# Optimization experiments

Measured on AMD Instinct MI355X. Metric: run time of the kernel, lower is better.

## Reference

```python
import jax, jax.numpy as jnp
import numpy as np

BS, C_IN, CTX, TGT = 2, 8, 1024, 96
D_MODEL, N_HEADS, D_FF, N_LAYERS = 256, 16, 1024, 4
PF, SF, PC, SC = 8, 4, 32, 16
NF = (CTX + SF - PF) // SF + 1   # 256 fine patches (incl. end-pad)
NC = (CTX + SC - PC) // SC + 1   # 64 coarse patches
TOTAL = NF + NC                  # 320
EPS = 1e-5
DK = D_MODEL // N_HEADS
SCALE = DK ** -0.5


def _patchify(z, plen, stride):
    # ReplicationPad1d((0, stride)) then unfold -> (bs, c, n_patches, plen)
    pad = jnp.broadcast_to(z[..., -1:], z.shape[:-1] + (stride,))
    zp = jnp.concatenate([z, pad], axis=-1)
    n = (zp.shape[-1] - plen) // stride + 1
    idx = np.arange(n)[:, None] * stride + np.arange(plen)[None, :]
    return zp[..., idx]


def _layernorm(x, s, b):
    m = x.mean(-1, keepdims=True)
    v = jnp.var(x, axis=-1, keepdims=True)
    return (x - m) * jax.lax.rsqrt(v + EPS) * s + b


def setup_inputs() -> dict:
    key = jax.random.key(0)
    ks = jax.random.split(key, 16)
    g = lambda k, shape: jax.random.normal(k, shape, jnp.float32) * 0.02
    return {
        "z": jax.random.normal(ks[0], (BS, C_IN, CTX), jnp.float32),
        "revin_w": jnp.ones((C_IN,), jnp.float32),
        "revin_b": jnp.zeros((C_IN,), jnp.float32),
        "Wf": g(ks[1], (PF, D_MODEL)), "bf": jnp.zeros((D_MODEL,), jnp.float32),
        "Wc": g(ks[2], (PC, D_MODEL)), "bc": jnp.zeros((D_MODEL,), jnp.float32),
        "W_pos": jax.random.uniform(ks[3], (TOTAL, D_MODEL), jnp.float32, -0.02, 0.02),
        "WQ": g(ks[4], (N_LAYERS, D_MODEL, D_MODEL)), "bQ": jnp.zeros((N_LAYERS, D_MODEL), jnp.float32),
        "WK": g(ks[5], (N_LAYERS, D_MODEL, D_MODEL)), "bK": jnp.zeros((N_LAYERS, D_MODEL), jnp.float32),
        "WV": g(ks[6], (N_LAYERS, D_MODEL, D_MODEL)), "bV": jnp.zeros((N_LAYERS, D_MODEL), jnp.float32),
        "WO": g(ks[7], (N_LAYERS, D_MODEL, D_MODEL)), "bO": jnp.zeros((N_LAYERS, D_MODEL), jnp.float32),
        "ln1_s": jnp.ones((N_LAYERS, D_MODEL), jnp.float32), "ln1_b": jnp.zeros((N_LAYERS, D_MODEL), jnp.float32),
        "ln2_s": jnp.ones((N_LAYERS, D_MODEL), jnp.float32), "ln2_b": jnp.zeros((N_LAYERS, D_MODEL), jnp.float32),
        "F1": g(ks[8], (N_LAYERS, D_MODEL, D_FF)), "c1": jnp.zeros((N_LAYERS, D_FF), jnp.float32),
        "F2": g(ks[9], (N_LAYERS, D_FF, D_MODEL)), "c2": jnp.zeros((N_LAYERS, D_MODEL), jnp.float32),
        "Wh": g(ks[10], (D_MODEL * TOTAL, TGT)), "bh": jnp.zeros((TGT,), jnp.float32),
    }


def reference(z, revin_w, revin_b, Wf, bf, Wc, bc, W_pos, WQ, bQ, WK, bK, WV, bV,
              WO, bO, ln1_s, ln1_b, ln2_s, ln2_b, F1, c1, F2, c2, Wh, bh):
    # RevIN norm over the time axis (last axis of (bs, c, T))
    mean = z.mean(-1, keepdims=True)
    std = jnp.sqrt(jnp.var(z, axis=-1, keepdims=True) + EPS)
    zn = (z - mean) / std * revin_w[None, :, None] + revin_b[None, :, None]

    # dual-scale patch embedding
    x_fine = _patchify(zn, PF, SF) @ Wf + bf      # (bs, c, NF, d)
    x_coarse = _patchify(zn, PC, SC) @ Wc + bc    # (bs, c, NC, d)
    x = jnp.concatenate([x_fine, x_coarse], axis=2)  # (bs, c, TOTAL, d)

    u = x.reshape(BS * C_IN, TOTAL, D_MODEL) + W_pos  # (B, S, d), B=bs*c

    # residual-score transformer encoder (post-norm)
    prev = None
    for l in range(N_LAYERS):
        q = (u @ WQ[l] + bQ[l]).reshape(-1, TOTAL, N_HEADS, DK).transpose(0, 2, 1, 3)
        k = (u @ WK[l] + bK[l]).reshape(-1, TOTAL, N_HEADS, DK).transpose(0, 2, 1, 3)
        v = (u @ WV[l] + bV[l]).reshape(-1, TOTAL, N_HEADS, DK).transpose(0, 2, 1, 3)
        s = jnp.einsum('bhqd,bhkd->bhqk', q, k) * SCALE
        if prev is not None:
            s = s + prev
        w = jax.nn.softmax(s, axis=-1)
        o = jnp.einsum('bhqk,bhkd->bhqd', w, v).transpose(0, 2, 1, 3).reshape(-1, TOTAL, D_MODEL)
        o = o @ WO[l] + bO[l]
        u = _layernorm(u + o, ln1_s[l], ln1_b[l])
        h = jax.nn.gelu(u @ F1[l] + c1[l], approximate=False) @ F2[l] + c2[l]
        u = _layernorm(u + h, ln2_s[l], ln2_b[l])
        prev = s

    # head: (bs, c, TOTAL, d) -> permute -> flatten(d, TOTAL) -> linear
    zz = u.reshape(BS, C_IN, TOTAL, D_MODEL).transpose(0, 1, 3, 2).reshape(BS, C_IN, D_MODEL * TOTAL)
    out = zz @ Wh + bh  # (bs, c, TGT)

    # RevIN denorm
    out = (out - revin_b[None, :, None]) / (revin_w[None, :, None] + EPS * EPS) * std + mean
    return out
```

## Files before the change

kernel.cpp:

```cpp
#include <hip/hip_runtime.h>
#include <math.h>

typedef unsigned short ushort;
typedef unsigned int uint;
typedef __attribute__((ext_vector_type(8))) short short8;
typedef __attribute__((ext_vector_type(4))) float f32x4;
typedef __attribute__((ext_vector_type(4))) ushort us4;

constexpr int BS = 2, C_IN = 8, CTX = 1024, TGT = 96;
constexpr int DM = 256, NH = 16, DFF = 1024, NL = 4;
constexpr int NF = 256, TOTAL = 320;
constexpr int NB = 16;
constexpr int DK = 16;
constexpr float EPS = 1e-5f;
constexpr float SCALE = 0.25f;
constexpr int KHEAD = DM * TOTAL;
constexpr int M = NB * TOTAL;

__device__ __forceinline__ ushort f2b(float x) {
    uint u = __float_as_uint(x);
    u += 0x7fff + ((u >> 16) & 1);
    return (ushort)(u >> 16);
}
__device__ __forceinline__ float bu2f(ushort x) { return __uint_as_float(((uint)x) << 16); }
__device__ __forceinline__ float lo2f(uint p) { return __uint_as_float(p << 16); }
__device__ __forceinline__ float hi2f(uint p) { return __uint_as_float(p & 0xffff0000u); }
__device__ __forceinline__ uint pack2(float a, float b) { return (uint)f2b(a) | ((uint)f2b(b) << 16); }

__global__ void k_convt(const float* __restrict__ src, ushort* __restrict__ dst,
                        int R, int C, int sls, int dls) {
    __shared__ ushort tile[32][33];
    src += (size_t)blockIdx.z * sls;
    dst += (size_t)blockIdx.z * dls;
    int c0 = blockIdx.x * 32, r0 = blockIdx.y * 32;
    int tx = threadIdx.x, ty = threadIdx.y;
    tile[ty][tx] = f2b(src[(r0 + ty) * C + c0 + tx]);
    __syncthreads();
    dst[(c0 + ty) * R + r0 + tx] = tile[tx][ty];
}

__global__ void k_convt_sq(const float* __restrict__ WQ, const float* __restrict__ WK,
                           const float* __restrict__ WV, const float* __restrict__ WO,
                           ushort* __restrict__ Wtqkv, ushort* __restrict__ WtO) {
    __shared__ ushort tile[32][33];
    int z = blockIdx.z, w = z >> 2, l = z & 3;
    const float* src = (w == 0 ? WQ : (w == 1 ? WK : (w == 2 ? WV : WO))) + l * 65536;
    ushort* dst = (w < 3) ? (Wtqkv + (size_t)l * 768 * 256 + w * 256 * 256)
                          : (WtO + (size_t)l * 65536);
    int c0 = blockIdx.x * 32, r0 = blockIdx.y * 32;
    int tx = threadIdx.x, ty = threadIdx.y;
    tile[ty][tx] = f2b(src[(r0 + ty) * 256 + c0 + tx]);
    __syncthreads();
    dst[(c0 + ty) * 256 + r0 + tx] = tile[tx][ty];
}

__global__ void k_convt_head(const float* __restrict__ Wh, ushort* __restrict__ WhT2) {
    __shared__ ushort tile[32][33];
    int t0 = blockIdx.x * 32, d0 = blockIdx.y * 32, p = blockIdx.z;
    int tx = threadIdx.x, ty = threadIdx.y;
    tile[ty][tx] = f2b(Wh[((size_t)(d0 + ty) * 320 + p) * 96 + t0 + tx]);
    __syncthreads();
    WhT2[(size_t)(t0 + ty) * KHEAD + p * 256 + d0 + tx] = tile[tx][ty];
}

__global__ void k_revin(const float* __restrict__ z, const float* __restrict__ rw,
                        const float* __restrict__ rb, float* __restrict__ zn,
                        float* __restrict__ meanv, float* __restrict__ stdv) {
    int bc = blockIdx.x, t = threadIdx.x;
    __shared__ float r1[256], r2[256];
    float s1 = 0.f, s2 = 0.f;
    for (int i = t; i < CTX; i += 256) {
        float x = z[bc * CTX + i];
        s1 += x; s2 += x * x;
    }
    r1[t] = s1; r2[t] = s2; __syncthreads();
    for (int off = 128; off > 0; off >>= 1) {
        if (t < off) { r1[t] += r1[t + off]; r2[t] += r2[t + off]; }
        __syncthreads();
    }
    float m = r1[0] * (1.0f / CTX);
    float var = r2[0] * (1.0f / CTX) - m * m;
    float sd = sqrtf(var + EPS);
    float w = rw[bc % C_IN], b = rb[bc % C_IN];
    float inv = 1.0f / sd;
    for (int i = t; i < CTX; i += 256) {
        float x = z[bc * CTX + i];
        zn[bc * CTX + i] = (x - m) * inv * w + b;
    }
    if (t == 0) { meanv[bc] = m; stdv[bc] = sd; }
}

__global__ void k_embed(const float* __restrict__ zn, const float* __restrict__ Wf,
                        const float* __restrict__ bfv, const float* __restrict__ Wc,
                        const float* __restrict__ bcv, const float* __restrict__ Wpos,
                        ushort* __restrict__ u) {
    int bc = blockIdx.x / TOTAL, p = blockIdx.x % TOTAL, d = threadIdx.x;
    float acc;
    if (p < NF) {
        acc = bfv[d];
        int base = p * 4;
        for (int i = 0; i < 8; i++) {
            int idx = min(base + i, CTX - 1);
            acc += zn[bc * CTX + idx] * Wf[i * DM + d];
        }
    } else {
        int pc = p - NF;
        acc = bcv[d];
        int base = pc * 16;
        for (int i = 0; i < 32; i++) {
            int idx = min(base + i, CTX - 1);
            acc += zn[bc * CTX + idx] * Wc[i * DM + d];
        }
    }
    acc += Wpos[p * DM + d];
    u[(bc * TOTAL + p) * DM + d] = f2b(acc);
}

template <int GELU, int QKV>
__global__ __launch_bounds__(256) void k_gemm_mfma(const ushort* __restrict__ A,
                                                   const ushort* __restrict__ Wt,
                                                   const float* __restrict__ b0,
                                                   const float* __restrict__ b1,
                                                   const float* __restrict__ b2,
                                                   ushort* __restrict__ C,
                                                   int Mm, int N, int K) {
    __shared__ ushort As[64][40];
    __shared__ ushort Bs[64][40];
    int tid = threadIdx.x;
    int wave = tid >> 6, lane = tid & 63;
    int quad = lane >> 4, l16 = lane & 15;
    int m0 = blockIdx.y * 64, n0 = blockIdx.x * 64;

    f32x4 acc[4];
#pragma unroll
    for (int nt = 0; nt < 4; nt++) acc[nt] = (f32x4){0.f, 0.f, 0.f, 0.f};

    int row = tid >> 2, kc = (tid & 3) * 8;
    for (int k0 = 0; k0 < K; k0 += 32) {
        *(short8*)&As[row][kc] = *(const short8*)&A[(m0 + row) * K + k0 + kc];
        *(short8*)&Bs[row][kc] = *(const short8*)&Wt[(n0 + row) * K + k0 + kc];
        __syncthreads();
        short8 af = *(const short8*)&As[wave * 16 + l16][quad * 8];
#pragma unroll
        for (int nt = 0; nt < 4; nt++) {
            short8 bf = *(const short8*)&Bs[nt * 16 + l16][quad * 8];
            acc[nt] = __builtin_amdgcn_mfma_f32_16x16x32_bf16(af, bf, acc[nt], 0, 0, 0);
        }
        __syncthreads();
    }
#pragma unroll
    for (int nt = 0; nt < 4; nt++) {
        int col = n0 + nt * 16 + l16;
        float bi;
        if (QKV) {
            int bs = (n0 + nt * 16) >> 8;
            const float* bp = bs == 0 ? b0 : (bs == 1 ? b1 : b2);
            bi = bp[col & 255];
        } else {
            bi = b0[col];
        }
#pragma unroll
        for (int r = 0; r < 4; r++) {
            int rowm = m0 + wave * 16 + quad * 4 + r;
            float vv = acc[nt][r] + bi;
            if (GELU) vv = vv * 0.5f * (1.0f + erff(vv * 0.70710678118f));
            if (QKV) C[(col >> 8) * (M * DM) + rowm * DM + (col & 255)] = f2b(vv);
            else C[rowm * N + col] = f2b(vv);
        }
    }
}

__global__ __launch_bounds__(256, 4) void k_attn(const ushort* __restrict__ qm, const ushort* __restrict__ km,
                                                 const ushort* __restrict__ vm, uint4* __restrict__ sp,
                                                 ushort* __restrict__ ao, int mode) {
    __shared__ ushort sh[10240];
    uint* sh32 = (uint*)sh;
    int bh = blockIdx.x, b = bh >> 4, h = bh & 15;
    int i0 = blockIdx.y * 64;
    int t = threadIdx.x, wave = t >> 6, lane = t & 63, quad = lane >> 4, l16 = lane & 15;
    const short8 zero8 = (short8){0, 0, 0, 0, 0, 0, 0, 0};

    for (int idx = t; idx < 640; idx += 256) {
        int j = idx >> 1, half = idx & 1;
        short8 kv = *(const short8*)&km[(b * TOTAL + j) * DM + h * DK + half * 8];
        int jt = j >> 4, jl = j & 15;
        *(short8*)&sh[((jt * 2 + half) * 16 + jl) * 8] = kv;
    }
    for (int idx = t; idx < 320; idx += 256) {
        int jp = idx >> 1, dh = idx & 1;
        int j = jp * 2;
        uint4 a = *(const uint4*)&vm[(b * TOTAL + j) * DM + h * DK + dh * 8];
        uint4 bb = *(const uint4*)&vm[(b * TOTAL + j + 1) * DM + h * DK + dh * 8];
        const ushort* ap = (const ushort*)&a;
        const ushort* bp = (const ushort*)&bb;
        int jr = j & 31;
        int q = (jr & 15) >> 2, jj = ((jr >> 4) << 2) + (jr & 3);
        int base = 5120 + ((j >> 5) * 4 + q) * 128 + jj;
#pragma unroll
        for (int dd = 0; dd < 8; dd++) {
            int d = dh * 8 + dd;
            uint val = (uint)ap[dd] | ((uint)bp[dd] << 16);
            sh32[(base + d * 8) >> 1] = val;
        }
    }
    short8 qf = zero8;
    if (quad < 2) qf = *(const short8*)&qm[(b * TOTAL + i0 + wave * 16 + l16) * DM + h * DK + quad * 8];
    __syncthreads();

    f32x4 acc[20];
#pragma unroll
    for (int nt = 0; nt < 20; nt++) {
        short8 kf = *(const short8*)&sh[((nt * 2 + (quad & 1)) * 16 + l16) * 8];
        acc[nt] = __builtin_amdgcn_mfma_f32_16x16x32_bf16(kf, qf, (f32x4){0.f, 0.f, 0.f, 0.f}, 0, 0, 0);
    }

    int cb = (bh * 5 + (int)blockIdx.y) * 10 * 256 + t;
#pragma unroll
    for (int c = 0; c < 10; c++) {
        float e[8];
#pragma unroll
        for (int j = 0; j < 8; j++) e[j] = acc[2 * c + (j >> 2)][j & 3] * SCALE;
        if (mode) {
            uint4 pv = sp[cb + c * 256];
            e[0] += lo2f(pv.x); e[1] += hi2f(pv.x); e[2] += lo2f(pv.y); e[3] += hi2f(pv.y);
            e[4] += lo2f(pv.z); e[5] += hi2f(pv.z); e[6] += lo2f(pv.w); e[7] += hi2f(pv.w);
        }
        if (mode != 2) {
            uint4 ov;
            ov.x = pack2(e[0], e[1]); ov.y = pack2(e[2], e[3]);
            ov.z = pack2(e[4], e[5]); ov.w = pack2(e[6], e[7]);
            sp[cb + c * 256] = ov;
        }
#pragma unroll
        for (int j = 0; j < 8; j++) acc[2 * c + (j >> 2)][j & 3] = e[j];
    }

    float mx = -1e30f;
#pragma unroll
    for (int nt = 0; nt < 20; nt++)
#pragma unroll
        for (int r = 0; r < 4; r++) mx = fmaxf(mx, acc[nt][r]);
    mx = fmaxf(mx, __shfl_xor(mx, 16));
    mx = fmaxf(mx, __shfl_xor(mx, 32));
    float sum = 0.f;
#pragma unroll
    for (int nt = 0; nt < 20; nt++)
#pragma unroll
        for (int r = 0; r < 4; r++) { acc[nt][r] = __expf(acc[nt][r] - mx); sum += acc[nt][r]; }
    sum += __shfl_xor(sum, 16);
    sum += __shfl_xor(sum, 32);
    float inv = 1.f / sum;
#pragma unroll
    for (int nt = 0; nt < 20; nt++)
#pragma unroll
        for (int r = 0; r < 4; r++) acc[nt][r] *= inv;

    f32x4 oacc = (f32x4){0.f, 0.f, 0.f, 0.f};
#pragma unroll
    for (int jt2 = 0; jt2 < 10; jt2++) {
        short8 vt = *(const short8*)&sh[5120 + ((jt2 * 4 + quad) * 16 + l16) * 8];
        union { short8 v; uint u[4]; } pf;
        pf.u[0] = pack2(acc[2 * jt2][0], acc[2 * jt2][1]);
        pf.u[1] = pack2(acc[2 * jt2][2], acc[2 * jt2][3]);
        pf.u[2] = pack2(acc[2 * jt2 + 1][0], acc[2 * jt2 + 1][1]);
        pf.u[3] = pack2(acc[2 * jt2 + 1][2], acc[2 * jt2 + 1][3]);
        oacc = __builtin_amdgcn_mfma_f32_16x16x32_bf16(vt, pf.v, oacc, 0, 0, 0);
    }
    us4 ov4 = (us4){f2b(oacc[0]), f2b(oacc[1]), f2b(oacc[2]), f2b(oacc[3])};
    *(us4*)&ao[(b * TOTAL + i0 + wave * 16 + l16) * DM + h * DK + quad * 4] = ov4;
}

__global__ __launch_bounds__(256) void k_add_ln(ushort* __restrict__ u, const ushort* __restrict__ o,
                                                const float* __restrict__ ls, const float* __restrict__ lb) {
    int wave = threadIdx.x >> 6, lane = threadIdx.x & 63;
    int row = blockIdx.x * 4 + wave;
    int d0 = lane * 4;
    uint2 uv = *(const uint2*)&u[row * DM + d0];
    uint2 ov = *(const uint2*)&o[row * DM + d0];
    float x0 = lo2f(uv.x) + lo2f(ov.x);
    float x1 = hi2f(uv.x) + hi2f(ov.x);
    float x2 = lo2f(uv.y) + lo2f(ov.y);
    float x3 = hi2f(uv.y) + hi2f(ov.y);
    float sum = x0 + x1 + x2 + x3;
    float sq = x0 * x0 + x1 * x1 + x2 * x2 + x3 * x3;
#pragma unroll
    for (int off = 1; off < 64; off <<= 1) {
        sum += __shfl_xor(sum, off);
        sq += __shfl_xor(sq, off);
    }
    float m = sum * (1.0f / DM);
    float var = sq * (1.0f / DM) - m * m;
    float rs = rsqrtf(var + EPS);
    f32x4 sc = *(const f32x4*)&ls[d0];
    f32x4 bb = *(const f32x4*)&lb[d0];
    float y0 = (x0 - m) * rs * sc[0] + bb[0];
    float y1 = (x1 - m) * rs * sc[1] + bb[1];
    float y2 = (x2 - m) * rs * sc[2] + bb[2];
    float y3 = (x3 - m) * rs * sc[3] + bb[3];
    uint2 w;
    w.x = pack2(y0, y1); w.y = pack2(y2, y3);
    *(uint2*)&u[row * DM + d0] = w;
}

__global__ __launch_bounds__(256) void k_head(const ushort* __restrict__ u, const ushort* __restrict__ WhT2,
                                              float* __restrict__ acc_head) {
    int t0 = blockIdx.x * 16;
    int wave = threadIdx.x >> 6, lane = threadIdx.x & 63;
    int quad = lane >> 4, l16 = lane & 15;
    int kbeg = (blockIdx.y * 4 + wave) * 1024;
    f32x4 acc = (f32x4){0.f, 0.f, 0.f, 0.f};
    const ushort* za = &u[(size_t)l16 * KHEAD + quad * 8];
    const ushort* wb = &WhT2[(size_t)(t0 + l16) * KHEAD + quad * 8];
#pragma unroll 4
    for (int k = kbeg; k < kbeg + 1024; k += 32) {
        short8 af = *(const short8*)&za[k];
        short8 bf = *(const short8*)&wb[k];
        acc = __builtin_amdgcn_mfma_f32_16x16x32_bf16(af, bf, acc, 0, 0, 0);
    }
#pragma unroll
    for (int r = 0; r < 4; r++)
        atomicAdd(&acc_head[(quad * 4 + r) * TGT + t0 + l16], acc[r]);
}

__global__ void k_final(const float* __restrict__ acc_head, const float* __restrict__ bh,
                        const float* __restrict__ rw, const float* __restrict__ rb,
                        const float* __restrict__ meanv, const float* __restrict__ stdv,
                        float* __restrict__ out) {
    int idx = blockIdx.x * 256 + threadIdx.x;
    if (idx >= NB * TGT) return;
    int bc = idx / TGT, t = idx % TGT, c = bc % C_IN;
    float vv = acc_head[idx] + bh[t];
    vv = (vv - rb[c]) / (rw[c] + EPS * EPS) * stdv[bc] + meanv[bc];
    out[idx] = vv;
}

extern "C" void kernel_launch(void* const* d_in, const int* in_sizes, int n_in,
                              void* d_out, int out_size, void* d_ws, size_t ws_size,
                              hipStream_t stream) {
    const float* z       = (const float*)d_in[0];
    const float* revin_w = (const float*)d_in[1];
    const float* revin_b = (const float*)d_in[2];
    const float* Wf      = (const float*)d_in[3];
    const float* bfv     = (const float*)d_in[4];
    const float* Wc      = (const float*)d_in[5];
    const float* bcv     = (const float*)d_in[6];
    const float* Wpos    = (const float*)d_in[7];
    const float* WQ      = (const float*)d_in[8];
    const float* bQ      = (const float*)d_in[9];
    const float* WK      = (const float*)d_in[10];
    const float* bK      = (const float*)d_in[11];
    const float* WV      = (const float*)d_in[12];
    const float* bV      = (const float*)d_in[13];
    const float* WO      = (const float*)d_in[14];
    const float* bO      = (const float*)d_in[15];
    const float* ln1s    = (const float*)d_in[16];
    const float* ln1b    = (const float*)d_in[17];
    const float* ln2s    = (const float*)d_in[18];
    const float* ln2b    = (const float*)d_in[19];
    const float* F1      = (const float*)d_in[20];
    const float* c1      = (const float*)d_in[21];
    const float* F2      = (const float*)d_in[22];
    const float* c2      = (const float*)d_in[23];
    const float* Wh      = (const float*)d_in[24];
    const float* bh      = (const float*)d_in[25];
    float* out = (float*)d_out;

    char* p = (char*)d_ws;
    float* meanv = (float*)p;    p += 16 * 4;
    float* stdv  = (float*)p;    p += 16 * 4;
    float* acc_head = (float*)p; p += NB * TGT * 4;
    p = (char*)(((size_t)p + 255) & ~255ull);
    float* zn = (float*)p;       p += NB * CTX * 4;
    ushort* u    = (ushort*)p;   p += (size_t)M * DM * 2;
    ushort* qkv  = (ushort*)p;   p += (size_t)3 * M * DM * 2;
    ushort* ax   = (ushort*)p;   p += (size_t)M * DM * 2;
    ushort* o    = (ushort*)p;   p += (size_t)M * DM * 2;
    ushort* hbuf = (ushort*)p;   p += (size_t)M * DFF * 2;
    ushort* Wtqkv = (ushort*)p;  p += (size_t)NL * 768 * 256 * 2;
    ushort* WtO   = (ushort*)p;  p += (size_t)NL * 256 * 256 * 2;
    ushort* Ft1   = (ushort*)p;  p += (size_t)NL * 1024 * 256 * 2;
    ushort* Ft2   = (ushort*)p;  p += (size_t)NL * 256 * 1024 * 2;
    ushort* WhT2  = (ushort*)p;  p += (size_t)TGT * KHEAD * 2;
    p = (char*)(((size_t)p + 255) & ~255ull);
    uint4* sp = (uint4*)p;       p += (size_t)NB * NH * 5 * 10 * 256 * 16;

    k_convt_sq<<<dim3(8, 8, 16), dim3(32, 32), 0, stream>>>(WQ, WK, WV, WO, Wtqkv, WtO);
    k_convt<<<dim3(32, 8, 4), dim3(32, 32), 0, stream>>>(F1, Ft1, 256, 1024, 262144, 262144);
    k_convt<<<dim3(8, 32, 4), dim3(32, 32), 0, stream>>>(F2, Ft2, 1024, 256, 262144, 262144);
    k_convt_head<<<dim3(3, 8, 320), dim3(32, 32), 0, stream>>>(Wh, WhT2);

    k_revin<<<NB, 256, 0, stream>>>(z, revin_w, revin_b, zn, meanv, stdv);
    k_embed<<<NB * TOTAL, 256, 0, stream>>>(zn, Wf, bfv, Wc, bcv, Wpos, u);

    for (int l = 0; l < NL; l++) {
        int mode = (l == 0) ? 0 : (l == NL - 1 ? 2 : 1);
        k_gemm_mfma<0, 1><<<dim3(12, 80), 256, 0, stream>>>(
            u, Wtqkv + (size_t)l * 768 * 256, bQ + l * DM, bK + l * DM, bV + l * DM, qkv, M, 768, 256);
        k_attn<<<dim3(NB * NH, 5), 256, 0, stream>>>(qkv, qkv + M * DM, qkv + 2 * M * DM, sp, ax, mode);
        k_gemm_mfma<0, 0><<<dim3(4, 80), 256, 0, stream>>>(
            ax, WtO + (size_t)l * 65536, bO + l * DM, bO + l * DM, bO + l * DM, o, M, 256, 256);
        k_add_ln<<<M / 4, 256, 0, stream>>>(u, o, ln1s + l * DM, ln1b + l * DM);
        k_gemm_mfma<1, 0><<<dim3(16, 80), 256, 0, stream>>>(
            u, Ft1 + (size_t)l * 262144, c1 + l * DFF, c1, c1, hbuf, M, 1024, 256);
        k_gemm_mfma<0, 0><<<dim3(4, 80), 256, 0, stream>>>(
            hbuf, Ft2 + (size_t)l * 262144, c2 + l * DM, c2, c2, o, M, 256, 1024);
        k_add_ln<<<M / 4, 256, 0, stream>>>(u, o, ln2s + l * DM, ln2b + l * DM);
    }

    hipMemsetAsync(acc_head, 0, NB * TGT * sizeof(float), stream);
    k_head<<<dim3(TGT / 16, 20), 256, 0, stream>>>(u, WhT2, acc_head);
    k_final<<<(NB * TGT + 255) / 256, 256, 0, stream>>>(acc_head, bh, revin_w, revin_b, meanv, stdv, out);
}
```

Before: 498.3 us.

## Fuse output/FFN2 GEMMs with residual LayerNorm and merge weight prep kernels

Adds a GEMM kernel that computes a full 16-row by 256-column tile per block, then applies bias, the residual add and LayerNorm in the epilogue, replacing the separate GEMM plus add_ln pair after attention and after the FFN. The four weight transpose/convert kernels are merged into one launch, attention mode becomes a template parameter, and the head's atomics plus memset are replaced by per-chunk partial sums reduced in k_final. This cuts kernel launches and the round trip of the intermediate output buffer. The cost is that the fused GEMM runs only 320 blocks, each reloading the whole weight panel per K step, which may lower GEMM efficiency, especially for the K=1024 FFN2.

```diff
diff --git a/kernel.cpp b/kernel.cpp
--- a/kernel.cpp
+++ b/kernel.cpp
@@ -27,40 +27,49 @@
 __device__ __forceinline__ float hi2f(uint p) { return __uint_as_float(p & 0xffff0000u); }
 __device__ __forceinline__ uint pack2(float a, float b) { return (uint)f2b(a) | ((uint)f2b(b) << 16); }
 
-__global__ void k_convt(const float* __restrict__ src, ushort* __restrict__ dst,
-                        int R, int C, int sls, int dls) {
+__global__ void k_prep(const float* __restrict__ WQ, const float* __restrict__ WK,
+                       const float* __restrict__ WV, const float* __restrict__ WO,
+                       const float* __restrict__ F1, const float* __restrict__ F2,
+                       const float* __restrict__ Wh,
+                       ushort* __restrict__ Wtqkv, ushort* __restrict__ WtO,
+                       ushort* __restrict__ Ft1, ushort* __restrict__ Ft2,
+                       ushort* __restrict__ WhT2) {
     __shared__ ushort tile[32][33];
-    src += (size_t)blockIdx.z * sls;
-    dst += (size_t)blockIdx.z * dls;
-    int c0 = blockIdx.x * 32, r0 = blockIdx.y * 32;
+    int i = blockIdx.x;
     int tx = threadIdx.x, ty = threadIdx.y;
-    tile[ty][tx] = f2b(src[(r0 + ty) * C + c0 + tx]);
-    __syncthreads();
-    dst[(c0 + ty) * R + r0 + tx] = tile[tx][ty];
-}
-
-__global__ void k_convt_sq(const float* __restrict__ WQ, const float* __restrict__ WK,
-                           const float* __restrict__ WV, const float* __restrict__ WO,
-                           ushort* __restrict__ Wtqkv, ushort* __restrict__ WtO) {
-    __shared__ ushort tile[32][33];
-    int z = blockIdx.z, w = z >> 2, l = z & 3;
-    const float* src = (w == 0 ? WQ : (w == 1 ? WK : (w == 2 ? WV : WO))) + l * 65536;
-    ushort* dst = (w < 3) ? (Wtqkv + (size_t)l * 768 * 256 + w * 256 * 256)
-                          : (WtO + (size_t)l * 65536);
-    int c0 = blockIdx.x * 32, r0 = blockIdx.y * 32;
-    int tx = threadIdx.x, ty = threadIdx.y;
-    tile[ty][tx] = f2b(src[(r0 + ty) * 256 + c0 + tx]);
-    __syncthreads();
-    dst[(c0 + ty) * 256 + r0 + tx] = tile[tx][ty];
-}
-
-__global__ void k_convt_head(const float* __restrict__ Wh, ushort* __restrict__ WhT2) {
-    __shared__ ushort tile[32][33];
-    int t0 = blockIdx.x * 32, d0 = blockIdx.y * 32, p = blockIdx.z;
-    int tx = threadIdx.x, ty = threadIdx.y;
-    tile[ty][tx] = f2b(Wh[((size_t)(d0 + ty) * 320 + p) * 96 + t0 + tx]);
-    __syncthreads();
-    WhT2[(size_t)(t0 + ty) * KHEAD + p * 256 + d0 + tx] = tile[tx][ty];
+    if (i < 1024) {
+        int z = i >> 6, w = z >> 2, l = z & 3;
+        const float* src = (w == 0 ? WQ : (w == 1 ? WK : (w == 2 ? WV : WO))) + l * 65536;
+        ushort* dst = (w < 3) ? (Wtqkv + (size_t)l * 768 * 256 + w * 256 * 256)
+                              : (WtO + (size_t)l * 65536);
+        int c0 = (i & 7) * 32, r0 = ((i >> 3) & 7) * 32;
+        tile[ty][tx] = f2b(src[(r0 + ty) * 256 + c0 + tx]);
+        __syncthreads();
+        dst[(c0 + ty) * 256 + r0 + tx] = tile[tx][ty];
+    } else if (i < 2048) {
+        int j = i - 1024, l = j >> 8;
+        const float* src = F1 + (size_t)l * 262144;
+        ushort* dst = Ft1 + (size_t)l * 262144;
+        int c0 = (j & 31) * 32, r0 = ((j >> 5) & 7) * 32;
+        tile[ty][tx] = f2b(src[(r0 + ty) * 1024 + c0 + tx]);
+        __syncthreads();
+        dst[(c0 + ty) * 256 + r0 + tx] = tile[tx][ty];
+    } else if (i < 3072) {
+        int j = i - 2048, l = j >> 8;
+        const float* src = F2 + (size_t)l * 262144;
+        ushort* dst = Ft2 + (size_t)l * 262144;
+        int c0 = (j & 7) * 32, r0 = ((j >> 3) & 31) * 32;
+        tile[ty][tx] = f2b(src[(r0 + ty) * 256 + c0 + tx]);
+        __syncthreads();
+        dst[(c0 + ty) * 1024 + r0 + tx] = tile[tx][ty];
+    } else {
+        int j = i - 3072;
+        int t0 = (j % 3) * 32, rest = j / 3;
+        int d0 = (rest & 7) * 32, pp = rest >> 3;
+        tile[ty][tx] = f2b(Wh[((size_t)(d0 + ty) * 320 + pp) * 96 + t0 + tx]);
+        __syncthreads();
+        WhT2[(size_t)(t0 + ty) * KHEAD + pp * 256 + d0 + tx] = tile[tx][ty];
+    }
 }
 
 __global__ void k_revin(const float* __restrict__ z, const float* __restrict__ rw,
@@ -170,9 +179,77 @@
     }
 }
 
+__global__ __launch_bounds__(256) void k_gemm_ln16(const ushort* __restrict__ A,
+                                                   const ushort* __restrict__ Wt,
+                                                   const float* __restrict__ bias,
+                                                   const float* __restrict__ ls,
+                                                   const float* __restrict__ lb,
+                                                   ushort* __restrict__ u, int K) {
+    __shared__ ushort As[16][40];
+    __shared__ ushort Bs[256][40];
+    __shared__ float ps1[16][4], ps2[16][4];
+    int tid = threadIdx.x;
+    int wave = tid >> 6, lane = tid & 63;
+    int quad = lane >> 4, l16 = lane & 15;
+    int m0 = blockIdx.x * 16;
+
+    f32x4 acc[4];
+#pragma unroll
+    for (int nt = 0; nt < 4; nt++) acc[nt] = (f32x4){0.f, 0.f, 0.f, 0.f};
+
+    int row = tid >> 2, kc = (tid & 3) * 8;
+    for (int k0 = 0; k0 < K; k0 += 32) {
+        if (tid < 64) *(short8*)&As[row][kc] = *(const short8*)&A[(m0 + row) * K + k0 + kc];
+#pragma unroll
+        for (int i = 0; i < 4; i++)
+            *(short8*)&Bs[i * 64 + row][kc] = *(const short8*)&Wt[(i * 64 + row) * K + k0 + kc];
+        __syncthreads();
+        short8 af = *(const short8*)&As[l16][quad * 8];
+#pragma unroll
+        for (int nt = 0; nt < 4; nt++) {
+            short8 bf = *(const short8*)&Bs[wave * 64 + nt * 16 + l16][quad * 8];
+            acc[nt] = __builtin_amdgcn_mfma_f32_16x16x32_bf16(af, bf, acc[nt], 0, 0, 0);
+        }
+        __syncthreads();
+    }
+    float xv[4][4];
+#pragma unroll
+    for (int r = 0; r < 4; r++) {
+        int rowg = m0 + quad * 4 + r;
+        float s1 = 0.f, s2 = 0.f;
+#pragma unroll
+        for (int nt = 0; nt < 4; nt++) {
+            int col = wave * 64 + nt * 16 + l16;
+            float x = acc[nt][r] + bias[col] + bu2f(u[rowg * DM + col]);
+            xv[r][nt] = x; s1 += x; s2 += x * x;
+        }
+        s1 += __shfl_xor(s1, 1); s2 += __shfl_xor(s2, 1);
+        s1 += __shfl_xor(s1, 2); s2 += __shfl_xor(s2, 2);
+        s1 += __shfl_xor(s1, 4); s2 += __shfl_xor(s2, 4);
+        s1 += __shfl_xor(s1, 8); s2 += __shfl_xor(s2, 8);
+        if (l16 == 0) { ps1[quad * 4 + r][wave] = s1; ps2[quad * 4 + r][wave] = s2; }
+    }
+    __syncthreads();
+#pragma unroll
+    for (int r = 0; r < 4; r++) {
+        int rowl = quad * 4 + r, rowg = m0 + rowl;
+        float s1 = ps1[rowl][0] + ps1[rowl][1] + ps1[rowl][2] + ps1[rowl][3];
+        float s2 = ps2[rowl][0] + ps2[rowl][1] + ps2[rowl][2] + ps2[rowl][3];
+        float m = s1 * (1.0f / DM);
+        float var = s2 * (1.0f / DM) - m * m;
+        float rs = rsqrtf(var + EPS);
+#pragma unroll
+        for (int nt = 0; nt < 4; nt++) {
+            int col = wave * 64 + nt * 16 + l16;
+            u[rowg * DM + col] = f2b((xv[r][nt] - m) * rs * ls[col] + lb[col]);
+        }
+    }
+}
+
+template <int MODE>
 __global__ __launch_bounds__(256, 4) void k_attn(const ushort* __restrict__ qm, const ushort* __restrict__ km,
                                                  const ushort* __restrict__ vm, uint4* __restrict__ sp,
-                                                 ushort* __restrict__ ao, int mode) {
+                                                 ushort* __restrict__ ao) {
     __shared__ ushort sh[10240];
     uint* sh32 = (uint*)sh;
     int bh = blockIdx.x, b = bh >> 4, h = bh & 15;
@@ -220,12 +297,12 @@
         float e[8];
 #pragma unroll
         for (int j = 0; j < 8; j++) e[j] = acc[2 * c + (j >> 2)][j & 3] * SCALE;
-        if (mode) {
+        if (MODE) {
             uint4 pv = sp[cb + c * 256];
             e[0] += lo2f(pv.x); e[1] += hi2f(pv.x); e[2] += lo2f(pv.y); e[3] += hi2f(pv.y);
             e[4] += lo2f(pv.z); e[5] += hi2f(pv.z); e[6] += lo2f(pv.w); e[7] += hi2f(pv.w);
         }
-        if (mode != 2) {
+        if (MODE != 2) {
             uint4 ov;
             ov.x = pack2(e[0], e[1]); ov.y = pack2(e[2], e[3]);
             ov.z = pack2(e[4], e[5]); ov.w = pack2(e[6], e[7]);
@@ -270,44 +347,13 @@
     *(us4*)&ao[(b * TOTAL + i0 + wave * 16 + l16) * DM + h * DK + quad * 4] = ov4;
 }
 
-__global__ __launch_bounds__(256) void k_add_ln(ushort* __restrict__ u, const ushort* __restrict__ o,
-                                                const float* __restrict__ ls, const float* __restrict__ lb) {
-    int wave = threadIdx.x >> 6, lane = threadIdx.x & 63;
-    int row = blockIdx.x * 4 + wave;
-    int d0 = lane * 4;
-    uint2 uv = *(const uint2*)&u[row * DM + d0];
-    uint2 ov = *(const uint2*)&o[row * DM + d0];
-    float x0 = lo2f(uv.x) + lo2f(ov.x);
-    float x1 = hi2f(uv.x) + hi2f(ov.x);
-    float x2 = lo2f(uv.y) + lo2f(ov.y);
-    float x3 = hi2f(uv.y) + hi2f(ov.y);
-    float sum = x0 + x1 + x2 + x3;
-    float sq = x0 * x0 + x1 * x1 + x2 * x2 + x3 * x3;
-#pragma unroll
-    for (int off = 1; off < 64; off <<= 1) {
-        sum += __shfl_xor(sum, off);
-        sq += __shfl_xor(sq, off);
-    }
-    float m = sum * (1.0f / DM);
-    float var = sq * (1.0f / DM) - m * m;
-    float rs = rsqrtf(var + EPS);
-    f32x4 sc = *(const f32x4*)&ls[d0];
-    f32x4 bb = *(const f32x4*)&lb[d0];
-    float y0 = (x0 - m) * rs * sc[0] + bb[0];
-    float y1 = (x1 - m) * rs * sc[1] + bb[1];
-    float y2 = (x2 - m) * rs * sc[2] + bb[2];
-    float y3 = (x3 - m) * rs * sc[3] + bb[3];
-    uint2 w;
-    w.x = pack2(y0, y1); w.y = pack2(y2, y3);
-    *(uint2*)&u[row * DM + d0] = w;
-}
-
 __global__ __launch_bounds__(256) void k_head(const ushort* __restrict__ u, const ushort* __restrict__ WhT2,
-                                              float* __restrict__ acc_head) {
+                                              float* __restrict__ part) {
     int t0 = blockIdx.x * 16;
     int wave = threadIdx.x >> 6, lane = threadIdx.x & 63;
     int quad = lane >> 4, l16 = lane & 15;
-    int kbeg = (blockIdx.y * 4 + wave) * 1024;
+    int chunk = blockIdx.y * 4 + wave;
+    int kbeg = chunk * 1024;
     f32x4 acc = (f32x4){0.f, 0.f, 0.f, 0.f};
     const ushort* za = &u[(size_t)l16 * KHEAD + quad * 8];
     const ushort* wb = &WhT2[(size_t)(t0 + l16) * KHEAD + quad * 8];
@@ -319,17 +365,18 @@
     }
 #pragma unroll
     for (int r = 0; r < 4; r++)
-        atomicAdd(&acc_head[(quad * 4 + r) * TGT + t0 + l16], acc[r]);
-}
-
-__global__ void k_final(const float* __restrict__ acc_head, const float* __restrict__ bh,
+        part[(size_t)chunk * (NB * TGT) + (quad * 4 + r) * TGT + t0 + l16] = acc[r];
+}
+
+__global__ void k_final(const float* __restrict__ part, const float* __restrict__ bh,
                         const float* __restrict__ rw, const float* __restrict__ rb,
                         const float* __restrict__ meanv, const float* __restrict__ stdv,
                         float* __restrict__ out) {
     int idx = blockIdx.x * 256 + threadIdx.x;
     if (idx >= NB * TGT) return;
     int bc = idx / TGT, t = idx % TGT, c = bc % C_IN;
-    float vv = acc_head[idx] + bh[t];
+    float vv = bh[t];
+    for (int j = 0; j < 80; j++) vv += part[(size_t)j * (NB * TGT) + idx];
     vv = (vv - rb[c]) / (rw[c] + EPS * EPS) * stdv[bc] + meanv[bc];
     out[idx] = vv;
 }
@@ -368,13 +415,12 @@
     char* p = (char*)d_ws;
     float* meanv = (float*)p;    p += 16 * 4;
     float* stdv  = (float*)p;    p += 16 * 4;
-    float* acc_head = (float*)p; p += NB * TGT * 4;
     p = (char*)(((size_t)p + 255) & ~255ull);
+    float* part = (float*)p;     p += (size_t)80 * NB * TGT * 4;
     float* zn = (float*)p;       p += NB * CTX * 4;
     ushort* u    = (ushort*)p;   p += (size_t)M * DM * 2;
     ushort* qkv  = (ushort*)p;   p += (size_t)3 * M * DM * 2;
     ushort* ax   = (ushort*)p;   p += (size_t)M * DM * 2;
-    ushort* o    = (ushort*)p;   p += (size_t)M * DM * 2;
     ushort* hbuf = (ushort*)p;   p += (size_t)M * DFF * 2;
     ushort* Wtqkv = (ushort*)p;  p += (size_t)NL * 768 * 256 * 2;
     ushort* WtO   = (ushort*)p;  p += (size_t)NL * 256 * 256 * 2;
@@ -384,30 +430,28 @@
     p = (char*)(((size_t)p + 255) & ~255ull);
     uint4* sp = (uint4*)p;       p += (size_t)NB * NH * 5 * 10 * 256 * 16;
 
-    k_convt_sq<<<dim3(8, 8, 16), dim3(32, 32), 0, stream>>>(WQ, WK, WV, WO, Wtqkv, WtO);
-    k_convt<<<dim3(32, 8, 4), dim3(32, 32), 0, stream>>>(F1, Ft1, 256, 1024, 262144, 262144);
-    k_convt<<<dim3(8, 32, 4), dim3(32, 32), 0, stream>>>(F2, Ft2, 1024, 256, 262144, 262144);
-    k_convt_head<<<dim3(3, 8, 320), dim3(32, 32), 0, stream>>>(Wh, WhT2);
-
+    k_prep<<<10752, dim3(32, 32), 0, stream>>>(WQ, WK, WV, WO, F1, F2, Wh,
+                                               Wtqkv, WtO, Ft1, Ft2, WhT2);
     k_revin<<<NB, 256, 0, stream>>>(z, revin_w, revin_b, zn, meanv, stdv);
     k_embed<<<NB * TOTAL, 256, 0, stream>>>(zn, Wf, bfv, Wc, bcv, Wpos, u);
 
     for (int l = 0; l < NL; l++) {
-        int mode = (l == 0) ? 0 : (l == NL - 1 ? 2 : 1);
         k_gemm_mfma<0, 1><<<dim3(12, 80), 256, 0, stream>>>(
             u, Wtqkv + (size_t)l * 768 * 256, bQ + l * DM, bK + l * DM, bV + l * DM, qkv, M, 768, 256);
-        k_attn<<<dim3(NB * NH, 5), 256, 0, stream>>>(qkv, qkv + M * DM, qkv + 2 * M * DM, sp, ax, mode);
-        k_gemm_mfma<0, 0><<<dim3(4, 80), 256, 0, stream>>>(
-            ax, WtO + (size_t)l * 65536, bO + l * DM, bO + l * DM, bO + l * DM, o, M, 256, 256);
-        k_add_ln<<<M / 4, 256, 0, stream>>>(u, o, ln1s + l * DM, ln1b + l * DM);
+        if (l == 0)
+            k_attn<0><<<dim3(NB * NH, 5), 256, 0, stream>>>(qkv, qkv + M * DM, qkv + 2 * M * DM, sp, ax);
+        else if (l == NL - 1)
+            k_attn<2><<<dim3(NB * NH, 5), 256, 0, stream>>>(qkv, qkv + M * DM, qkv + 2 * M * DM, sp, ax);
+        else
+            k_attn<1><<<dim3(NB * NH, 5), 256, 0, stream>>>(qkv, qkv + M * DM, qkv + 2 * M * DM, sp, ax);
+        k_gemm_ln16<<<M / 16, 256, 0, stream>>>(
+            ax, WtO + (size_t)l * 65536, bO + l * DM, ln1s + l * DM, ln1b + l * DM, u, 256);
         k_gemm_mfma<1, 0><<<dim3(16, 80), 256, 0, stream>>>(
             u, Ft1 + (size_t)l * 262144, c1 + l * DFF, c1, c1, hbuf, M, 1024, 256);
-        k_gemm_mfma<0, 0><<<dim3(4, 80), 256, 0, stream>>>(
-            hbuf, Ft2 + (size_t)l * 262144, c2 + l * DM, c2, c2, o, M, 256, 1024);
-        k_add_ln<<<M / 4, 256, 0, stream>>>(u, o, ln2s + l * DM, ln2b + l * DM);
-    }
-
-    hipMemsetAsync(acc_head, 0, NB * TGT * sizeof(float), stream);
-    k_head<<<dim3(TGT / 16, 20), 256, 0, stream>>>(u, WhT2, acc_head);
-    k_final<<<(NB * TGT + 255) / 256, 256, 0, stream>>>(acc_head, bh, revin_w, revin_b, meanv, stdv, out);
-}
+        k_gemm_ln16<<<M / 16, 256, 0, stream>>>(
+            hbuf, Ft2 + (size_t)l * 262144, c2 + l * DM, ln2s + l * DM, ln2b + l * DM, u, 1024);
+    }
+
+    k_head<<<dim3(TGT / 16, 20), 256, 0, stream>>>(u, WhT2, part);
+    k_final<<<(NB * TGT + 255) / 256, 256, 0, stream>>>(part, bh, revin_w, revin_b, meanv, stdv, out);
+}
```

Result: no change. 505.9 us (+1.5%).
